# Optimization experiments

Hardware: AMD Instinct MI355X
Metric: run time of the kernel (lower is better)

The kernel has to match this reference:

```python
import jax, jax.numpy as jnp
import numpy as np

B, T, C, H, N = 2, 1024, 1024, 16, 64
D_DECAY, D_AAA, D_MV, D_GATE = 64, 64, 32, 128
LN_EPS = 64e-5  # GroupNorm eps used by RWKV7 (1e-5 * head_size_divisor**2)


def setup_inputs():
    key = jax.random.key(0)
    ks = jax.random.split(key, 32)
    rn = lambda k, shape, s=1.0: jax.random.normal(k, shape, jnp.float32) * s
    p = {}
    p['x'] = rn(ks[0], (B, T, C))
    p['v_first'] = rn(ks[1], (B, T, C))
    for i, nm in enumerate(['x_r', 'x_w', 'x_k', 'x_v', 'x_a', 'x_g']):
        p[nm] = jax.random.uniform(ks[2 + i], (1, 1, C), jnp.float32)
    p['w1'] = rn(ks[8], (C, D_DECAY), 0.02); p['w2'] = rn(ks[9], (D_DECAY, C), 0.02); p['w0'] = rn(ks[10], (C,), 0.5)
    p['a1'] = rn(ks[11], (C, D_AAA), 0.02); p['a2'] = rn(ks[12], (D_AAA, C), 0.02); p['a0'] = rn(ks[13], (C,), 0.1)
    p['v1'] = rn(ks[14], (C, D_MV), 0.02); p['v2'] = rn(ks[15], (D_MV, C), 0.02); p['v0'] = rn(ks[16], (C,), 0.1)
    p['g1'] = rn(ks[17], (C, D_GATE), 0.02); p['g2'] = rn(ks[18], (D_GATE, C), 0.02)
    p['k_k'] = jax.random.uniform(ks[19], (1, 1, C), jnp.float32)
    p['k_a'] = jax.random.uniform(ks[20], (1, 1, C), jnp.float32)
    p['r_k'] = rn(ks[21], (H, N), 0.1)
    s = C ** -0.5
    p['W_r'] = rn(ks[22], (C, C), s); p['W_k'] = rn(ks[23], (C, C), s)
    p['W_v'] = rn(ks[24], (C, C), s); p['W_o'] = rn(ks[25], (C, C), s)
    p['ln_w'] = jnp.ones((C,), jnp.float32); p['ln_b'] = jnp.zeros((C,), jnp.float32)
    return p


def _rwkv7_op(r, w, k, v, a, b):
    # r,w,k,v,a,b: (B,T,C). Per-head matrix-state recurrence:
    #   S_t = S_{t-1} * diag(decay_t) + (S_{t-1} @ a_t) b_t^T + v_t k_t^T ; out_t = S_t @ r_t
    f = lambda z: z.reshape(B, T, H, N).astype(jnp.float32).transpose(1, 0, 2, 3)  # (T,B,H,N)
    r_, k_, v_, a_, b_ = f(r), f(k), f(v), f(a), f(b)
    d_ = jnp.exp(-jnp.exp(f(w)))  # decay in (0,1)

    def step(S, inp):
        rt, dt, kt, vt, at, bt = inp  # each (B,H,N)
        sa = jnp.einsum('bhij,bhj->bhi', S, at)
        S = S * dt[:, :, None, :] + sa[..., None] * bt[:, :, None, :] + vt[..., None] * kt[:, :, None, :]
        return S, jnp.einsum('bhij,bhj->bhi', S, rt)

    S0 = jnp.zeros((B, H, N, N), jnp.float32)
    _, out = jax.lax.scan(step, S0, (r_, d_, k_, v_, a_, b_))
    return out.transpose(1, 0, 2, 3).reshape(B, T, C)


def _forward(x, v_first, x_r, x_w, x_k, x_v, x_a, x_g, w1, w2, w0, a1, a2, a0,
             v1, v2, v0, g1, g2, k_k, k_a, r_k, W_r, W_k, W_v, W_o, ln_w, ln_b):
    xx = jnp.pad(x, ((0, 0), (1, 0), (0, 0)))[:, :T] - x  # token shift
    xr = x + xx * x_r; xw = x + xx * x_w; xk = x + xx * x_k
    xv = x + xx * x_v; xa = x + xx * x_a; xg = x + xx * x_g
    r = xr @ W_r
    w = -jax.nn.softplus(-(jnp.tanh(xw @ w1) @ w2 + w0)) - 0.5
    k = xk @ W_k
    v = xv @ W_v
    v = v + (v_first - v) * jax.nn.sigmoid(xv @ v1 @ v2 + v0)  # layer_id > 0 branch
    a = jax.nn.sigmoid(xa @ a1 @ a2 + a0)
    g = jax.nn.sigmoid(xg @ g1) @ g2
    kk = (k * k_k).reshape(B, T, H, N)
    kk = (kk / jnp.maximum(jnp.linalg.norm(kk, axis=-1, keepdims=True), 1e-12)).reshape(B, T, C)
    k = k * (1.0 + (a - 1.0) * k_a)
    y = _rwkv7_op(r, w, k, v, -kk, kk * a)
    # GroupNorm(H groups over C) applied per token
    yh = y.reshape(B, T, H, N)
    mu = yh.mean(-1, keepdims=True)
    var = yh.var(-1, keepdims=True)
    y = ((yh - mu) / jnp.sqrt(var + LN_EPS)).reshape(B, T, C) * ln_w + ln_b
    rh = r.reshape(B, T, H, N); kh = k.reshape(B, T, H, N); vh = v.reshape(B, T, H, N)
    y = y + ((rh * kh * r_k).sum(-1, keepdims=True) * vh).reshape(B, T, C)
    return (y * g) @ W_o


def reference(x, v_first, x_r, x_w, x_k, x_v, x_a, x_g, w1, w2, w0, a1, a2, a0,
              v1, v2, v0, g1, g2, k_k, k_a, r_k, W_r, W_k, W_v, W_o, ln_w, ln_b):
    out = _forward(x, v_first, x_r, x_w, x_k, x_v, x_a, x_g, w1, w2, w0, a1, a2, a0,
                   v1, v2, v0, g1, g2, k_k, k_a, r_k, W_r, W_k, W_v, W_o, ln_w, ln_b)
    return (out, v_first)
```

## Files before the change

### kernel.cpp

```cpp
#include <hip/hip_runtime.h>
#include <hip/hip_bf16.h>
#include <cstdint>
#include <cstddef>

typedef __hip_bfloat16 bf16;
typedef __bf16 bf16x8 __attribute__((ext_vector_type(8)));
typedef float f32x4 __attribute__((ext_vector_type(4)));

#define BB 2
#define TT 1024
#define CC 1024
#define HH 16
#define PKS 448
#define PKB 1792
#define CH 8
#define NCH 4
#define STEPB 2048
#define CHB (CH * STEPB)
#define NC (TT / CH)

__device__ __forceinline__ bf16 f2b(float v){ return __float2bfloat16(v); }

__device__ __forceinline__ float hex_add(float x) {
    x += __int_as_float(__builtin_amdgcn_mov_dpp(__float_as_int(x), 0xB1, 0xF, 0xF, true));
    x += __int_as_float(__builtin_amdgcn_mov_dpp(__float_as_int(x), 0x4E, 0xF, 0xF, true));
    x += __int_as_float(__builtin_amdgcn_mov_dpp(__float_as_int(x), 0x141, 0xF, 0xF, true));
    x += __int_as_float(__builtin_amdgcn_mov_dpp(__float_as_int(x), 0x140, 0xF, 0xF, true));
    return x;
}

typedef __attribute__((address_space(3))) void as3_void;
typedef __attribute__((address_space(1))) const void as1_void;
__device__ __forceinline__ void gload_lds16(const void* g, void* l) {
    __builtin_amdgcn_global_load_lds((as1_void*)g, (as3_void*)l, 16, 0, 0);
}

struct TrDesc { const float* in; bf16* out; int R, S; };
struct TrArgs { TrDesc d[12]; };

__global__ __launch_bounds__(256) void transpose_batch(TrArgs args)
{
    TrDesc t = args.d[blockIdx.z];
    __shared__ float tile[32][33];
    int s0 = blockIdx.x * 32, r0 = blockIdx.y * 32;
    if (s0 >= t.S || r0 >= t.R) return;
    int tx = threadIdx.x & 31, ty = threadIdx.x >> 5;
#pragma unroll
    for (int i = 0; i < 4; i++) {
        int r = r0 + ty + i * 8, s = s0 + tx;
        if (r < t.R && s < t.S) tile[ty + i * 8][tx] = t.in[(size_t)r * t.S + s];
    }
    __syncthreads();
#pragma unroll
    for (int i = 0; i < 4; i++) {
        int s = s0 + ty + i * 8, r = r0 + tx;
        if (s < t.S && r < t.R) t.out[(size_t)s * t.R + r] = f2b(tile[tx][ty + i * 8]);
    }
}

__global__ __launch_bounds__(256) void mix_kernel(
    const float* __restrict__ x, const float* __restrict__ vfirst,
    const float* __restrict__ mr, const float* __restrict__ mw, const float* __restrict__ mk,
    const float* __restrict__ mv, const float* __restrict__ ma, const float* __restrict__ mg,
    bf16* __restrict__ xr, bf16* __restrict__ xw, bf16* __restrict__ xk,
    bf16* __restrict__ xv, bf16* __restrict__ xa, bf16* __restrict__ xg,
    float* __restrict__ vout)
{
    int row = blockIdx.x;
    int t = row & (TT - 1);
    size_t base = (size_t)row * CC;
    for (int c = threadIdx.x; c < CC; c += 256) {
        float xc = x[base + c];
        float xp = (t > 0) ? x[base - CC + c] : 0.f;
        float d = xp - xc;
        xr[base + c] = f2b(xc + d * mr[c]);
        xw[base + c] = f2b(xc + d * mw[c]);
        xk[base + c] = f2b(xc + d * mk[c]);
        xv[base + c] = f2b(xc + d * mv[c]);
        xa[base + c] = f2b(xc + d * ma[c]);
        xg[base + c] = f2b(xc + d * mg[c]);
        vout[base + c] = vfirst[base + c];
    }
}

template <class EmitF>
__device__ __forceinline__ void gemm_tile(const bf16* __restrict__ A, const bf16* __restrict__ BT,
                                          int K, int m0, int n0, EmitF emit)
{
    __shared__ __align__(16) bf16 Atile[128 * 32];
    __shared__ __align__(16) bf16 Btile[128 * 32];
    int tid = threadIdx.x;
    int w = tid >> 6, lane = tid & 63;
    int wr = w >> 1, wc = w & 1;
    int quad = lane >> 4, l16 = lane & 15;

    f32x4 zero = {0.f, 0.f, 0.f, 0.f};
    f32x4 acc[4][4];
#pragma unroll
    for (int i = 0; i < 4; i++)
#pragma unroll
        for (int j = 0; j < 4; j++) acc[i][j] = zero;

    int rr = lane >> 2;
    int cs = lane & 3;
    int ra0 = w * 32 + rr;
    int ra1 = ra0 + 16;
    int cg0 = cs ^ ((ra0 >> 1) & 3);
    int cg1 = cs ^ ((ra1 >> 1) & 3);

    for (int k0 = 0; k0 < K; k0 += 32) {
        uint4 av0 = *reinterpret_cast<const uint4*>(A  + (size_t)(m0 + ra0) * K + k0 + cg0 * 8);
        uint4 av1 = *reinterpret_cast<const uint4*>(A  + (size_t)(m0 + ra1) * K + k0 + cg1 * 8);
        uint4 bv0 = *reinterpret_cast<const uint4*>(BT + (size_t)(n0 + ra0) * K + k0 + cg0 * 8);
        uint4 bv1 = *reinterpret_cast<const uint4*>(BT + (size_t)(n0 + ra1) * K + k0 + cg1 * 8);
        __syncthreads();
        *reinterpret_cast<uint4*>(&Atile[ra0 * 32 + cs * 8]) = av0;
        *reinterpret_cast<uint4*>(&Atile[ra1 * 32 + cs * 8]) = av1;
        *reinterpret_cast<uint4*>(&Btile[ra0 * 32 + cs * 8]) = bv0;
        *reinterpret_cast<uint4*>(&Btile[ra1 * 32 + cs * 8]) = bv1;
        __syncthreads();

        bf16x8 af[4], bfr[4];
#pragma unroll
        for (int mi = 0; mi < 4; mi++) {
            int m = wr * 64 + mi * 16 + l16;
            int c2 = quad ^ ((m >> 1) & 3);
            af[mi] = *reinterpret_cast<const bf16x8*>(&Atile[m * 32 + c2 * 8]);
        }
#pragma unroll
        for (int ni = 0; ni < 4; ni++) {
            int n = wc * 64 + ni * 16 + l16;
            int c2 = quad ^ ((n >> 1) & 3);
            bfr[ni] = *reinterpret_cast<const bf16x8*>(&Btile[n * 32 + c2 * 8]);
        }
#pragma unroll
        for (int mi = 0; mi < 4; mi++)
#pragma unroll
            for (int ni = 0; ni < 4; ni++)
                acc[mi][ni] = __builtin_amdgcn_mfma_f32_16x16x32_bf16(af[mi], bfr[ni], acc[mi][ni], 0, 0, 0);
    }

#pragma unroll
    for (int mi = 0; mi < 4; mi++)
#pragma unroll
        for (int ni = 0; ni < 4; ni++)
#pragma unroll
            for (int rg = 0; rg < 4; rg++) {
                int m = m0 + wr * 64 + mi * 16 + quad * 4 + rg;
                int n = n0 + wc * 64 + ni * 16 + l16;
                emit(m, n, acc[mi][ni][rg]);
            }
}

struct B3Args { const bf16* A[3]; const bf16* BT[3]; float* out[3]; };
__global__ __launch_bounds__(256) void big3_kernel(B3Args args)
{
    int z = blockIdx.z;
    float* out = args.out[z];
    gemm_tile(args.A[z], args.BT[z], 1024, blockIdx.x * 128, blockIdx.y * 128,
              [&](int m, int n, float v) { out[(size_t)m * 1024 + n] = v; });
}

struct L1Desc { const bf16* A; const bf16* BT; bf16* outB; int N; int mode; };
struct L1Args { L1Desc d[4]; };
__global__ __launch_bounds__(256) void lora1_kernel(L1Args args)
{
    L1Desc dz = args.d[blockIdx.z];
    gemm_tile(dz.A, dz.BT, 1024, blockIdx.x * 128, 0,
              [&](int m, int n, float v) {
                  if (n < dz.N) {
                      float r = (dz.mode == 2) ? tanhf(v)
                              : (dz.mode == 3) ? 1.f / (1.f + expf(-v)) : v;
                      dz.outB[(size_t)m * dz.N + n] = f2b(r);
                  }
              });
}

struct L2Desc { const bf16* A; const bf16* BT; const float* bias; float* outF; int K; int mode; };
struct L2Args { L2Desc d[4]; const float* vraw; const float* vfirst; };
__global__ __launch_bounds__(256) void lora2_kernel(L2Args args)
{
    L2Desc dz = args.d[blockIdx.z];
    gemm_tile(dz.A, dz.BT, dz.K, blockIdx.x * 128, blockIdx.y * 128,
              [&](int m, int n, float v) {
                  size_t idx = (size_t)m * 1024 + n;
                  if (dz.mode == 4) {
                      float xx = v + dz.bias[n];
                      float ww = -log1pf(expf(-xx)) - 0.5f;
                      dz.outF[idx] = expf(-expf(ww));
                  } else if (dz.mode == 5) {
                      float xx = v + dz.bias[n];
                      dz.outF[idx] = 1.f / (1.f + expf(-xx));
                  } else if (dz.mode == 6) {
                      float gate = 1.f / (1.f + expf(-(v + dz.bias[n])));
                      float vr = args.vraw[idx];
                      dz.outF[idx] = vr + (args.vfirst[idx] - vr) * gate;
                  } else {
                      dz.outF[idx] = v;
                  }
              });
}

__global__ __launch_bounds__(256) void final_kernel(const bf16* __restrict__ A, const bf16* __restrict__ BT,
                                                    float* __restrict__ out)
{
    gemm_tile(A, BT, 1024, blockIdx.x * 128, blockIdx.y * 128,
              [&](int m, int n, float v) { out[(size_t)m * 1024 + n] = v; });
}

__global__ __launch_bounds__(256) void pack_kernel(
    float* __restrict__ k, const float* __restrict__ a, const float* __restrict__ r,
    const float* __restrict__ v, const float* __restrict__ dw,
    const float* __restrict__ kkw, const float* __restrict__ kaw,
    float* __restrict__ PK)
{
    int tid = threadIdx.x;
    int wave = tid >> 6, lane = tid & 63;
    int idx = blockIdx.x * 4 + wave;
    size_t off = (size_t)idx * 64 + lane;
    int c = (idx & 15) * 64 + lane;
    float kraw = k[off];
    float av = a[off];
    float kkv = kraw * kkw[c];
    float s = kkv * kkv;
#pragma unroll
    for (int m = 32; m; m >>= 1) s += __shfl_xor(s, m);
    float kkn = kkv / fmaxf(sqrtf(s), 1e-12f);
    float ks = kraw * (1.f + (av - 1.f) * kaw[c]);
    k[off] = ks;
    float bb = kkn * av;
    float rv = r[off];
    float dv = dw[off];
    float bt = bb * rv, ct = ks * rv;
#pragma unroll
    for (int m = 32; m; m >>= 1) { bt += __shfl_xor(bt, m); ct += __shfl_xor(ct, m); }
    int b = idx >> 14;
    int h = idx & 15;
    int t = (idx >> 4) & (TT - 1);
    size_t sidx = (size_t)(b * HH + h) * TT + t;
    float* pw = PK + sidx * PKS;
    pw[lane] = ks; pw[64 + lane] = kkn; pw[128 + lane] = bb; pw[192 + lane] = v[off];
    pw[256 + lane] = rv; pw[320 + lane] = dv;
    if (lane == 0) { pw[384] = bt; pw[385] = ct; }
}

struct SetR { f32x4 q, d, r, k, b; float vi; float2 bc; };

__device__ __forceinline__ void ds_load_set(SetR& s, const char* slot, int c16, int row)
{
    s.q  = *(const f32x4*)(slot + 256  + c16);
    s.d  = *(const f32x4*)(slot + 1280 + c16);
    s.r  = *(const f32x4*)(slot + 1024 + c16);
    s.k  = *(const f32x4*)(slot + 0    + c16);
    s.b  = *(const f32x4*)(slot + 512  + c16);
    s.vi = *(const float*)(slot + 768 + row * 4);
    s.bc = *(const float2*)(slot + 1536);
}

__device__ __forceinline__ float step4(const SetR& sd, f32x4& S)
{
    f32x4 Sd   = S * sd.d;
    f32x4 sacv = S * sd.q;
    f32x4 oacv = Sd * sd.r;
    float sar = (sacv[0] + sacv[1]) + (sacv[2] + sacv[3]);
    float od  = (oacv[0] + oacv[1]) + (oacv[2] + oacv[3]);
    sar = hex_add(sar);
    od  = hex_add(od);
    float sa = -sar;
    float o = fmaf(sd.vi, sd.bc.y, fmaf(sa, sd.bc.x, od));
    S = Sd + sa * sd.b + sd.vi * sd.k;
    return o;
}

__global__ __launch_bounds__(256, 1) void scan_kernel(
    const float* __restrict__ PK, float* __restrict__ ybuf)
{
    __shared__ __align__(16) char ring[NCH * CHB];
    const int tid = threadIdx.x;
    const int wid = tid >> 6, lane = tid & 63;
    const int xcd = blockIdx.x & 7, kk = blockIdx.x >> 3;
    const int bh = xcd * 4 + (kk >> 4);
    const int wq = kk & 15;
    const int b = bh >> 4, h = bh & 15;
    const int row = wq * 4 + (lane >> 4);
    const int c = lane & 15;
    const int c16 = c * 16;

    const char* base = (const char*)(PK + (size_t)bh * TT * PKS);
    const char* g1 = base + lane * 16;
    const char* g2 = g1 + 1024;

    auto stage_chunk = [&](int ci) {
        const char* p1 = g1 + (size_t)ci * CH * PKB;
        const char* p2 = g2 + (size_t)ci * CH * PKB;
        char* s = ring + (ci & (NCH - 1)) * CHB;
        for (int j = wid - 1; j < CH; j += 3) {
            gload_lds16(p1 + (size_t)j * PKB, s + j * STEPB);
            gload_lds16(p2 + (size_t)j * PKB, s + j * STEPB + 1024);
        }
    };

    if (wid > 0) {
        stage_chunk(0);
        stage_chunk(1);
        stage_chunk(2);
    }
    __syncthreads();

    f32x4 S = {0.f, 0.f, 0.f, 0.f};
    SetR X, Y;
    if (wid == 0) ds_load_set(X, ring, c16, row);
    float* py = ybuf + (size_t)b * TT * CC + h * 64 + row;

    for (int i = 0; i < NC; i++) {
        if (wid == 0) {
            const char* sl  = ring + (i & (NCH - 1)) * CHB;
            const char* sln = ring + ((i + 1) & (NCH - 1)) * CHB;
            float o;
            ds_load_set(Y, sl + 1 * STEPB, c16, row); o = step4(X, S); if (c == 0) *py = o; py += CC;
            ds_load_set(X, sl + 2 * STEPB, c16, row); o = step4(Y, S); if (c == 0) *py = o; py += CC;
            ds_load_set(Y, sl + 3 * STEPB, c16, row); o = step4(X, S); if (c == 0) *py = o; py += CC;
            ds_load_set(X, sl + 4 * STEPB, c16, row); o = step4(Y, S); if (c == 0) *py = o; py += CC;
            ds_load_set(Y, sl + 5 * STEPB, c16, row); o = step4(X, S); if (c == 0) *py = o; py += CC;
            ds_load_set(X, sl + 6 * STEPB, c16, row); o = step4(Y, S); if (c == 0) *py = o; py += CC;
            ds_load_set(Y, sl + 7 * STEPB, c16, row); o = step4(X, S); if (c == 0) *py = o; py += CC;
            ds_load_set(X, sln,            c16, row); o = step4(Y, S); if (c == 0) *py = o; py += CC;
        } else {
            if (i + 3 < NC) stage_chunk(i + 3);
        }
        __syncthreads();
    }
}

__global__ __launch_bounds__(256) void gn_kernel(
    const float* __restrict__ y, const float* __restrict__ r, const float* __restrict__ k,
    const float* __restrict__ v, const float* __restrict__ g,
    const float* __restrict__ lnw, const float* __restrict__ lnb,
    const float* __restrict__ rk, bf16* __restrict__ z)
{
    int tid = threadIdx.x;
    int idx = blockIdx.x * 4 + (tid >> 6);
    int lane = tid & 63;
    size_t off = (size_t)idx * 64 + lane;
    int c = (idx & 15) * 64 + lane;
    float yv = y[off];
    float rv = r[off], kv = k[off], vv = v[off];
    float s1 = yv, s2 = yv * yv, s3 = rv * kv * rk[c];
#pragma unroll
    for (int m = 32; m; m >>= 1) {
        s1 += __shfl_xor(s1, m);
        s2 += __shfl_xor(s2, m);
        s3 += __shfl_xor(s3, m);
    }
    float mu = s1 * (1.f / 64.f);
    float var = fmaxf(s2 * (1.f / 64.f) - mu * mu, 0.f);
    float yn = (yv - mu) * rsqrtf(var + 64e-5f) * lnw[c] + lnb[c];
    float out = (yn + s3 * vv) * g[off];
    z[off] = f2b(out);
}

extern "C" void kernel_launch(void* const* d_in, const int* in_sizes, int n_in,
                              void* d_out, int out_size, void* d_ws, size_t ws_size,
                              hipStream_t stream)
{
    const float* x       = (const float*)d_in[0];
    const float* v_first = (const float*)d_in[1];
    const float* x_r = (const float*)d_in[2];
    const float* x_w = (const float*)d_in[3];
    const float* x_k = (const float*)d_in[4];
    const float* x_v = (const float*)d_in[5];
    const float* x_a = (const float*)d_in[6];
    const float* x_g = (const float*)d_in[7];
    const float* w1 = (const float*)d_in[8];
    const float* w2 = (const float*)d_in[9];
    const float* w0 = (const float*)d_in[10];
    const float* a1 = (const float*)d_in[11];
    const float* a2 = (const float*)d_in[12];
    const float* a0 = (const float*)d_in[13];
    const float* v1 = (const float*)d_in[14];
    const float* v2 = (const float*)d_in[15];
    const float* v0 = (const float*)d_in[16];
    const float* g1 = (const float*)d_in[17];
    const float* g2 = (const float*)d_in[18];
    const float* k_k = (const float*)d_in[19];
    const float* k_a = (const float*)d_in[20];
    const float* r_k = (const float*)d_in[21];
    const float* W_r = (const float*)d_in[22];
    const float* W_k = (const float*)d_in[23];
    const float* W_v = (const float*)d_in[24];
    const float* W_o = (const float*)d_in[25];
    const float* ln_w = (const float*)d_in[26];
    const float* ln_b = (const float*)d_in[27];

    const size_t BTC = (size_t)BB * TT * CC;
    const int M = BB * TT;

    char* ws = (char*)d_ws;
    size_t off = 0;
    auto alloc = [&](size_t bytes) -> char* {
        char* p = ws + off;
        off += (bytes + 255) & ~(size_t)255;
        return p;
    };

    bf16* xr = (bf16*)alloc(BTC * 2);
    bf16* xw = (bf16*)alloc(BTC * 2);
    bf16* xk = (bf16*)alloc(BTC * 2);
    bf16* xv = (bf16*)alloc(BTC * 2);
    bf16* xa = (bf16*)alloc(BTC * 2);
    bf16* xg = (bf16*)alloc(BTC * 2);
    bf16* WrT = (bf16*)alloc(1024 * 1024 * 2);
    bf16* WkT = (bf16*)alloc(1024 * 1024 * 2);
    bf16* WvT = (bf16*)alloc(1024 * 1024 * 2);
    bf16* w1T = (bf16*)alloc(128 * 1024 * 2);
    bf16* a1T = (bf16*)alloc(128 * 1024 * 2);
    bf16* v1T = (bf16*)alloc(128 * 1024 * 2);
    bf16* g1T = (bf16*)alloc(128 * 1024 * 2);
    bf16* w2T = (bf16*)alloc(1024 * 64 * 2);
    bf16* a2T = (bf16*)alloc(1024 * 64 * 2);
    bf16* v2T = (bf16*)alloc(1024 * 32 * 2);
    bf16* g2T = (bf16*)alloc(1024 * 128 * 2);
    bf16* h_w = (bf16*)alloc((size_t)M * 64 * 2);
    bf16* h_a = (bf16*)alloc((size_t)M * 64 * 2);
    bf16* h_v = (bf16*)alloc((size_t)M * 32 * 2);
    bf16* h_g = (bf16*)alloc((size_t)M * 128 * 2);

    float* PK = (float*)ws;
    size_t pk_end = (size_t)BB * HH * TT * PKS * 4;
    if (off < pk_end) off = pk_end;
    off = (off + 255) & ~(size_t)255;

    bf16* WoT = (bf16*)alloc(1024 * 1024 * 2);
    float* rbuf = (float*)alloc(BTC * 4);
    float* kbuf = (float*)alloc(BTC * 4);
    float* vraw = (float*)alloc(BTC * 4);
    float* vbuf = (float*)alloc(BTC * 4);
    float* dbuf = (float*)alloc(BTC * 4);
    float* abuf = (float*)alloc(BTC * 4);
    float* gbuf = (float*)alloc(BTC * 4);

    float* ybuf = vraw;
    bf16*  zbuf = (bf16*)dbuf;

    (void)in_sizes; (void)n_in; (void)out_size; (void)ws_size;

    TrArgs ta;
    ta.d[0]  = {W_r, WrT, 1024, 1024};
    ta.d[1]  = {W_k, WkT, 1024, 1024};
    ta.d[2]  = {W_v, WvT, 1024, 1024};
    ta.d[3]  = {W_o, WoT, 1024, 1024};
    ta.d[4]  = {w1, w1T, 1024, 64};
    ta.d[5]  = {a1, a1T, 1024, 64};
    ta.d[6]  = {v1, v1T, 1024, 32};
    ta.d[7]  = {g1, g1T, 1024, 128};
    ta.d[8]  = {w2, w2T, 64, 1024};
    ta.d[9]  = {a2, a2T, 64, 1024};
    ta.d[10] = {v2, v2T, 32, 1024};
    ta.d[11] = {g2, g2T, 128, 1024};
    transpose_batch<<<dim3(32, 32, 12), 256, 0, stream>>>(ta);

    float* vout = (float*)d_out + BTC;
    mix_kernel<<<BB * TT, 256, 0, stream>>>(x, v_first, x_r, x_w, x_k, x_v, x_a, x_g,
                                            xr, xw, xk, xv, xa, xg, vout);

    B3Args b3;
    b3.A[0] = xr; b3.A[1] = xk; b3.A[2] = xv;
    b3.BT[0] = WrT; b3.BT[1] = WkT; b3.BT[2] = WvT;
    b3.out[0] = rbuf; b3.out[1] = kbuf; b3.out[2] = vraw;
    big3_kernel<<<dim3(16, 8, 3), 256, 0, stream>>>(b3);

    L1Args l1;
    l1.d[0] = {xw, w1T, h_w, 64, 2};
    l1.d[1] = {xa, a1T, h_a, 64, 0};
    l1.d[2] = {xv, v1T, h_v, 32, 0};
    l1.d[3] = {xg, g1T, h_g, 128, 3};
    lora1_kernel<<<dim3(16, 1, 4), 256, 0, stream>>>(l1);

    L2Args l2;
    l2.d[0] = {h_w, w2T, w0, dbuf, 64, 4};
    l2.d[1] = {h_a, a2T, a0, abuf, 64, 5};
    l2.d[2] = {h_v, v2T, v0, vbuf, 32, 6};
    l2.d[3] = {h_g, g2T, nullptr, gbuf, 128, 0};
    l2.vraw = vraw; l2.vfirst = v_first;
    lora2_kernel<<<dim3(16, 8, 4), 256, 0, stream>>>(l2);

    pack_kernel<<<BB * TT * HH / 4, 256, 0, stream>>>(kbuf, abuf, rbuf, vbuf, dbuf, k_k, k_a, PK);

    scan_kernel<<<BB * HH * 16, 256, 0, stream>>>(PK, ybuf);

    gn_kernel<<<BB * TT * HH / 4, 256, 0, stream>>>(ybuf, rbuf, kbuf, vbuf, gbuf, ln_w, ln_b, r_k, zbuf);

    final_kernel<<<dim3(16, 8), 256, 0, stream>>>(zbuf, WoT, (float*)d_out);
}
```

Measured before the change: 431.7 us.

## Fuse transpose+mix, big3+lora1, and pack into scan staging

Merges the weight-transpose and token-mix kernels into one prep launch and the three big projections with the LoRA-down GEMMs into one proj launch. Removes the pack kernel and its packed intermediate buffer: each scan block now reads k, a, r, v and decay directly, computes the normalized kk, the adjusted k and the per-step dot products with wave reductions, and writes the results into its LDS ring. gn recomputes the adjusted k from a and k_a. This cuts launches and a full pack write/read round trip. In exchange, the scan's staging waves do more ALU and cross-lane reduction work, and the 16 row-blocks of each head repeat the same staging computation.

```diff
diff --git a/kernel.cpp b/kernel.cpp
--- a/kernel.cpp
+++ b/kernel.cpp
@@ -11,8 +11,6 @@
 #define TT 1024
 #define CC 1024
 #define HH 16
-#define PKS 448
-#define PKB 1792
 #define CH 8
 #define NCH 4
 #define STEPB 2048
@@ -29,57 +27,61 @@
     return x;
 }
 
-typedef __attribute__((address_space(3))) void as3_void;
-typedef __attribute__((address_space(1))) const void as1_void;
-__device__ __forceinline__ void gload_lds16(const void* g, void* l) {
-    __builtin_amdgcn_global_load_lds((as1_void*)g, (as3_void*)l, 16, 0, 0);
+__device__ __forceinline__ float red64(float x) {
+    x = hex_add(x);
+    x += __shfl_xor(x, 16);
+    x += __shfl_xor(x, 32);
+    return x;
 }
 
 struct TrDesc { const float* in; bf16* out; int R, S; };
-struct TrArgs { TrDesc d[12]; };
-
-__global__ __launch_bounds__(256) void transpose_batch(TrArgs args)
-{
-    TrDesc t = args.d[blockIdx.z];
-    __shared__ float tile[32][33];
-    int s0 = blockIdx.x * 32, r0 = blockIdx.y * 32;
-    if (s0 >= t.S || r0 >= t.R) return;
-    int tx = threadIdx.x & 31, ty = threadIdx.x >> 5;
-#pragma unroll
-    for (int i = 0; i < 4; i++) {
-        int r = r0 + ty + i * 8, s = s0 + tx;
-        if (r < t.R && s < t.S) tile[ty + i * 8][tx] = t.in[(size_t)r * t.S + s];
-    }
-    __syncthreads();
-#pragma unroll
-    for (int i = 0; i < 4; i++) {
-        int s = s0 + ty + i * 8, r = r0 + tx;
-        if (s < t.S && r < t.R) t.out[(size_t)s * t.R + r] = f2b(tile[tx][ty + i * 8]);
-    }
-}
-
-__global__ __launch_bounds__(256) void mix_kernel(
-    const float* __restrict__ x, const float* __restrict__ vfirst,
-    const float* __restrict__ mr, const float* __restrict__ mw, const float* __restrict__ mk,
-    const float* __restrict__ mv, const float* __restrict__ ma, const float* __restrict__ mg,
-    bf16* __restrict__ xr, bf16* __restrict__ xw, bf16* __restrict__ xk,
-    bf16* __restrict__ xv, bf16* __restrict__ xa, bf16* __restrict__ xg,
-    float* __restrict__ vout)
-{
-    int row = blockIdx.x;
-    int t = row & (TT - 1);
-    size_t base = (size_t)row * CC;
-    for (int c = threadIdx.x; c < CC; c += 256) {
-        float xc = x[base + c];
-        float xp = (t > 0) ? x[base - CC + c] : 0.f;
-        float d = xp - xc;
-        xr[base + c] = f2b(xc + d * mr[c]);
-        xw[base + c] = f2b(xc + d * mw[c]);
-        xk[base + c] = f2b(xc + d * mk[c]);
-        xv[base + c] = f2b(xc + d * mv[c]);
-        xa[base + c] = f2b(xc + d * ma[c]);
-        xg[base + c] = f2b(xc + d * mg[c]);
-        vout[base + c] = vfirst[base + c];
+struct PrepArgs {
+    TrDesc d[12];
+    const float* x; const float* vfirst;
+    const float *mr, *mw, *mk, *mv, *ma, *mg;
+    bf16 *xr, *xw, *xk, *xv, *xa, *xg;
+    float* vout;
+};
+
+__global__ __launch_bounds__(256) void prep_kernel(PrepArgs args)
+{
+    if (blockIdx.z < 12) {
+        TrDesc t = args.d[blockIdx.z];
+        __shared__ float tile[32][33];
+        int s0 = blockIdx.x * 32, r0 = blockIdx.y * 32;
+        if (s0 >= t.S || r0 >= t.R) return;
+        int tx = threadIdx.x & 31, ty = threadIdx.x >> 5;
+#pragma unroll
+        for (int i = 0; i < 4; i++) {
+            int r = r0 + ty + i * 8, s = s0 + tx;
+            if (r < t.R && s < t.S) tile[ty + i * 8][tx] = t.in[(size_t)r * t.S + s];
+        }
+        __syncthreads();
+#pragma unroll
+        for (int i = 0; i < 4; i++) {
+            int s = s0 + ty + i * 8, r = r0 + tx;
+            if (s < t.S && r < t.R) t.out[(size_t)s * t.R + r] = f2b(tile[tx][ty + i * 8]);
+        }
+        return;
+    }
+    int bid = blockIdx.y * 32 + blockIdx.x;
+#pragma unroll
+    for (int rr = 0; rr < 2; rr++) {
+        int row = bid * 2 + rr;
+        int t = row & (TT - 1);
+        size_t base = (size_t)row * CC;
+        for (int c = threadIdx.x; c < CC; c += 256) {
+            float xc = args.x[base + c];
+            float xp = (t > 0) ? args.x[base - CC + c] : 0.f;
+            float d = xp - xc;
+            args.xr[base + c] = f2b(xc + d * args.mr[c]);
+            args.xw[base + c] = f2b(xc + d * args.mw[c]);
+            args.xk[base + c] = f2b(xc + d * args.mk[c]);
+            args.xv[base + c] = f2b(xc + d * args.mv[c]);
+            args.xa[base + c] = f2b(xc + d * args.ma[c]);
+            args.xg[base + c] = f2b(xc + d * args.mg[c]);
+            args.vout[base + c] = args.vfirst[base + c];
+        }
     }
 }
 
@@ -152,20 +154,20 @@
             }
 }
 
-struct B3Args { const bf16* A[3]; const bf16* BT[3]; float* out[3]; };
-__global__ __launch_bounds__(256) void big3_kernel(B3Args args)
+struct L1Desc { const bf16* A; const bf16* BT; bf16* outB; int N; int mode; };
+struct ProjArgs { const bf16* A[3]; const bf16* BT[3]; float* out[3]; L1Desc d[4]; };
+
+__global__ __launch_bounds__(256) void proj_kernel(ProjArgs args)
 {
     int z = blockIdx.z;
-    float* out = args.out[z];
-    gemm_tile(args.A[z], args.BT[z], 1024, blockIdx.x * 128, blockIdx.y * 128,
-              [&](int m, int n, float v) { out[(size_t)m * 1024 + n] = v; });
-}
-
-struct L1Desc { const bf16* A; const bf16* BT; bf16* outB; int N; int mode; };
-struct L1Args { L1Desc d[4]; };
-__global__ __launch_bounds__(256) void lora1_kernel(L1Args args)
-{
-    L1Desc dz = args.d[blockIdx.z];
+    if (z < 3) {
+        float* out = args.out[z];
+        gemm_tile(args.A[z], args.BT[z], 1024, blockIdx.x * 128, blockIdx.y * 128,
+                  [&](int m, int n, float v) { out[(size_t)m * 1024 + n] = v; });
+        return;
+    }
+    if (blockIdx.y) return;
+    L1Desc dz = args.d[z - 3];
     gemm_tile(dz.A, dz.BT, 1024, blockIdx.x * 128, 0,
               [&](int m, int n, float v) {
                   if (n < dz.N) {
@@ -208,42 +210,6 @@
               [&](int m, int n, float v) { out[(size_t)m * 1024 + n] = v; });
 }
 
-__global__ __launch_bounds__(256) void pack_kernel(
-    float* __restrict__ k, const float* __restrict__ a, const float* __restrict__ r,
-    const float* __restrict__ v, const float* __restrict__ dw,
-    const float* __restrict__ kkw, const float* __restrict__ kaw,
-    float* __restrict__ PK)
-{
-    int tid = threadIdx.x;
-    int wave = tid >> 6, lane = tid & 63;
-    int idx = blockIdx.x * 4 + wave;
-    size_t off = (size_t)idx * 64 + lane;
-    int c = (idx & 15) * 64 + lane;
-    float kraw = k[off];
-    float av = a[off];
-    float kkv = kraw * kkw[c];
-    float s = kkv * kkv;
-#pragma unroll
-    for (int m = 32; m; m >>= 1) s += __shfl_xor(s, m);
-    float kkn = kkv / fmaxf(sqrtf(s), 1e-12f);
-    float ks = kraw * (1.f + (av - 1.f) * kaw[c]);
-    k[off] = ks;
-    float bb = kkn * av;
-    float rv = r[off];
-    float dv = dw[off];
-    float bt = bb * rv, ct = ks * rv;
-#pragma unroll
-    for (int m = 32; m; m >>= 1) { bt += __shfl_xor(bt, m); ct += __shfl_xor(ct, m); }
-    int b = idx >> 14;
-    int h = idx & 15;
-    int t = (idx >> 4) & (TT - 1);
-    size_t sidx = (size_t)(b * HH + h) * TT + t;
-    float* pw = PK + sidx * PKS;
-    pw[lane] = ks; pw[64 + lane] = kkn; pw[128 + lane] = bb; pw[192 + lane] = v[off];
-    pw[256 + lane] = rv; pw[320 + lane] = dv;
-    if (lane == 0) { pw[384] = bt; pw[385] = ct; }
-}
-
 struct SetR { f32x4 q, d, r, k, b; float vi; float2 bc; };
 
 __device__ __forceinline__ void ds_load_set(SetR& s, const char* slot, int c16, int row)
@@ -273,30 +239,45 @@
 }
 
 __global__ __launch_bounds__(256, 1) void scan_kernel(
-    const float* __restrict__ PK, float* __restrict__ ybuf)
+    const float* __restrict__ kb, const float* __restrict__ ab,
+    const float* __restrict__ rb, const float* __restrict__ vb,
+    const float* __restrict__ db, const float* __restrict__ kkw,
+    const float* __restrict__ kaw, float* __restrict__ ybuf)
 {
     __shared__ __align__(16) char ring[NCH * CHB];
     const int tid = threadIdx.x;
     const int wid = tid >> 6, lane = tid & 63;
-    const int xcd = blockIdx.x & 7, kk = blockIdx.x >> 3;
-    const int bh = xcd * 4 + (kk >> 4);
-    const int wq = kk & 15;
+    const int xcd = blockIdx.x & 7, kk2 = blockIdx.x >> 3;
+    const int bh = xcd * 4 + (kk2 >> 4);
+    const int wq = kk2 & 15;
     const int b = bh >> 4, h = bh & 15;
     const int row = wq * 4 + (lane >> 4);
     const int c = lane & 15;
     const int c16 = c * 16;
 
-    const char* base = (const char*)(PK + (size_t)bh * TT * PKS);
-    const char* g1 = base + lane * 16;
-    const char* g2 = g1 + 1024;
+    size_t ebase = (size_t)b * TT * CC + h * 64 + lane;
+    float kkw_l = kkw[h * 64 + lane];
+    float kaw_l = kaw[h * 64 + lane];
 
     auto stage_chunk = [&](int ci) {
-        const char* p1 = g1 + (size_t)ci * CH * PKB;
-        const char* p2 = g2 + (size_t)ci * CH * PKB;
-        char* s = ring + (ci & (NCH - 1)) * CHB;
         for (int j = wid - 1; j < CH; j += 3) {
-            gload_lds16(p1 + (size_t)j * PKB, s + j * STEPB);
-            gload_lds16(p2 + (size_t)j * PKB, s + j * STEPB + 1024);
+            size_t off = ebase + (size_t)(ci * CH + j) * CC;
+            float kv = kb[off], av = ab[off], rv = rb[off], vv = vb[off], dv = db[off];
+            float kkv = kv * kkw_l;
+            float ss  = red64(kkv * kkv);
+            float kkn = kkv / fmaxf(sqrtf(ss), 1e-12f);
+            float ks  = kv * fmaf(av - 1.f, kaw_l, 1.f);
+            float bbv = kkn * av;
+            float bt  = red64(bbv * rv);
+            float ct  = red64(ks * rv);
+            char* sp = ring + (ci & (NCH - 1)) * CHB + j * STEPB;
+            ((float*)(sp       ))[lane] = ks;
+            ((float*)(sp +  256))[lane] = kkn;
+            ((float*)(sp +  512))[lane] = bbv;
+            ((float*)(sp +  768))[lane] = vv;
+            ((float*)(sp + 1024))[lane] = rv;
+            ((float*)(sp + 1280))[lane] = dv;
+            if (lane == 0) { *(float*)(sp + 1536) = bt; *(float*)(sp + 1540) = ct; }
         }
     };
 
@@ -305,7 +286,9 @@
         stage_chunk(1);
         stage_chunk(2);
     }
-    __syncthreads();
+    asm volatile("s_waitcnt lgkmcnt(0)" ::: "memory");
+    __builtin_amdgcn_s_barrier();
+    __builtin_amdgcn_sched_barrier(0);
 
     f32x4 S = {0.f, 0.f, 0.f, 0.f};
     SetR X, Y;
@@ -328,15 +311,17 @@
         } else {
             if (i + 3 < NC) stage_chunk(i + 3);
         }
-        __syncthreads();
+        asm volatile("s_waitcnt lgkmcnt(0)" ::: "memory");
+        __builtin_amdgcn_s_barrier();
+        __builtin_amdgcn_sched_barrier(0);
     }
 }
 
 __global__ __launch_bounds__(256) void gn_kernel(
     const float* __restrict__ y, const float* __restrict__ r, const float* __restrict__ k,
-    const float* __restrict__ v, const float* __restrict__ g,
+    const float* __restrict__ a, const float* __restrict__ v, const float* __restrict__ g,
     const float* __restrict__ lnw, const float* __restrict__ lnb,
-    const float* __restrict__ rk, bf16* __restrict__ z)
+    const float* __restrict__ rk, const float* __restrict__ kaw, bf16* __restrict__ z)
 {
     int tid = threadIdx.x;
     int idx = blockIdx.x * 4 + (tid >> 6);
@@ -344,7 +329,8 @@
     size_t off = (size_t)idx * 64 + lane;
     int c = (idx & 15) * 64 + lane;
     float yv = y[off];
-    float rv = r[off], kv = k[off], vv = v[off];
+    float rv = r[off], vv = v[off];
+    float kv = k[off] * fmaf(a[off] - 1.f, kaw[c], 1.f);
     float s1 = yv, s2 = yv * yv, s3 = rv * kv * rk[c];
 #pragma unroll
     for (int m = 32; m; m >>= 1) {
@@ -424,12 +410,6 @@
     bf16* h_a = (bf16*)alloc((size_t)M * 64 * 2);
     bf16* h_v = (bf16*)alloc((size_t)M * 32 * 2);
     bf16* h_g = (bf16*)alloc((size_t)M * 128 * 2);
-
-    float* PK = (float*)ws;
-    size_t pk_end = (size_t)BB * HH * TT * PKS * 4;
-    if (off < pk_end) off = pk_end;
-    off = (off + 255) & ~(size_t)255;
-
     bf16* WoT = (bf16*)alloc(1024 * 1024 * 2);
     float* rbuf = (float*)alloc(BTC * 4);
     float* kbuf = (float*)alloc(BTC * 4);
@@ -444,37 +424,34 @@
 
     (void)in_sizes; (void)n_in; (void)out_size; (void)ws_size;
 
-    TrArgs ta;
-    ta.d[0]  = {W_r, WrT, 1024, 1024};
-    ta.d[1]  = {W_k, WkT, 1024, 1024};
-    ta.d[2]  = {W_v, WvT, 1024, 1024};
-    ta.d[3]  = {W_o, WoT, 1024, 1024};
-    ta.d[4]  = {w1, w1T, 1024, 64};
-    ta.d[5]  = {a1, a1T, 1024, 64};
-    ta.d[6]  = {v1, v1T, 1024, 32};
-    ta.d[7]  = {g1, g1T, 1024, 128};
-    ta.d[8]  = {w2, w2T, 64, 1024};
-    ta.d[9]  = {a2, a2T, 64, 1024};
-    ta.d[10] = {v2, v2T, 32, 1024};
-    ta.d[11] = {g2, g2T, 128, 1024};
-    transpose_batch<<<dim3(32, 32, 12), 256, 0, stream>>>(ta);
-
-    float* vout = (float*)d_out + BTC;
-    mix_kernel<<<BB * TT, 256, 0, stream>>>(x, v_first, x_r, x_w, x_k, x_v, x_a, x_g,
-                                            xr, xw, xk, xv, xa, xg, vout);
-
-    B3Args b3;
-    b3.A[0] = xr; b3.A[1] = xk; b3.A[2] = xv;
-    b3.BT[0] = WrT; b3.BT[1] = WkT; b3.BT[2] = WvT;
-    b3.out[0] = rbuf; b3.out[1] = kbuf; b3.out[2] = vraw;
-    big3_kernel<<<dim3(16, 8, 3), 256, 0, stream>>>(b3);
-
-    L1Args l1;
-    l1.d[0] = {xw, w1T, h_w, 64, 2};
-    l1.d[1] = {xa, a1T, h_a, 64, 0};
-    l1.d[2] = {xv, v1T, h_v, 32, 0};
-    l1.d[3] = {xg, g1T, h_g, 128, 3};
-    lora1_kernel<<<dim3(16, 1, 4), 256, 0, stream>>>(l1);
+    PrepArgs pa;
+    pa.d[0]  = {W_r, WrT, 1024, 1024};
+    pa.d[1]  = {W_k, WkT, 1024, 1024};
+    pa.d[2]  = {W_v, WvT, 1024, 1024};
+    pa.d[3]  = {W_o, WoT, 1024, 1024};
+    pa.d[4]  = {w1, w1T, 1024, 64};
+    pa.d[5]  = {a1, a1T, 1024, 64};
+    pa.d[6]  = {v1, v1T, 1024, 32};
+    pa.d[7]  = {g1, g1T, 1024, 128};
+    pa.d[8]  = {w2, w2T, 64, 1024};
+    pa.d[9]  = {a2, a2T, 64, 1024};
+    pa.d[10] = {v2, v2T, 32, 1024};
+    pa.d[11] = {g2, g2T, 128, 1024};
+    pa.x = x; pa.vfirst = v_first;
+    pa.mr = x_r; pa.mw = x_w; pa.mk = x_k; pa.mv = x_v; pa.ma = x_a; pa.mg = x_g;
+    pa.xr = xr; pa.xw = xw; pa.xk = xk; pa.xv = xv; pa.xa = xa; pa.xg = xg;
+    pa.vout = (float*)d_out + BTC;
+    prep_kernel<<<dim3(32, 32, 13), 256, 0, stream>>>(pa);
+
+    ProjArgs pj;
+    pj.A[0] = xr; pj.A[1] = xk; pj.A[2] = xv;
+    pj.BT[0] = WrT; pj.BT[1] = WkT; pj.BT[2] = WvT;
+    pj.out[0] = rbuf; pj.out[1] = kbuf; pj.out[2] = vraw;
+    pj.d[0] = {xw, w1T, h_w, 64, 2};
+    pj.d[1] = {xa, a1T, h_a, 64, 0};
+    pj.d[2] = {xv, v1T, h_v, 32, 0};
+    pj.d[3] = {xg, g1T, h_g, 128, 3};
+    proj_kernel<<<dim3(16, 8, 7), 256, 0, stream>>>(pj);
 
     L2Args l2;
     l2.d[0] = {h_w, w2T, w0, dbuf, 64, 4};
@@ -484,11 +461,10 @@
     l2.vraw = vraw; l2.vfirst = v_first;
     lora2_kernel<<<dim3(16, 8, 4), 256, 0, stream>>>(l2);
 
-    pack_kernel<<<BB * TT * HH / 4, 256, 0, stream>>>(kbuf, abuf, rbuf, vbuf, dbuf, k_k, k_a, PK);
-
-    scan_kernel<<<BB * HH * 16, 256, 0, stream>>>(PK, ybuf);
-
-    gn_kernel<<<BB * TT * HH / 4, 256, 0, stream>>>(ybuf, rbuf, kbuf, vbuf, gbuf, ln_w, ln_b, r_k, zbuf);
+    scan_kernel<<<BB * HH * 16, 256, 0, stream>>>(kbuf, abuf, rbuf, vbuf, dbuf, k_k, k_a, ybuf);
+
+    gn_kernel<<<BB * TT * HH / 4, 256, 0, stream>>>(ybuf, rbuf, kbuf, abuf, vbuf, gbuf,
+                                                    ln_w, ln_b, r_k, k_a, zbuf);
 
     final_kernel<<<dim3(16, 8), 256, 0, stream>>>(zbuf, WoT, (float*)d_out);
 }
```

Measured after the change: 514.5 us. 1.19x slower.
